# Kernel optimization log

Measured on AMD Instinct MI355X. Metric: run time of the kernel, lower is better.

## Reference

```python
import jax, jax.numpy as jnp
import numpy as np

NUM_USERS = 100000
NUM_ITEMS = 50000
N_TOTAL = NUM_USERS + NUM_ITEMS
NNZ = 4000000
LATENT_DIM = 64
N_LAYERS = 3
BATCH = 16384


def setup_inputs() -> dict:
    key = jax.random.key(0)
    k1, k2, k3, k4, k5, k6, k7 = jax.random.split(key, 7)
    return {
        "user_emb": jax.random.normal(k1, (NUM_USERS, LATENT_DIM), dtype=jnp.float32) * 0.1,
        "item_emb": jax.random.normal(k2, (NUM_ITEMS, LATENT_DIM), dtype=jnp.float32) * 0.1,
        "vals": jax.random.uniform(k3, (NNZ,), dtype=jnp.float32),
        "rows": jax.random.randint(k4, (NNZ,), 0, N_TOTAL, dtype=jnp.int32),
        "cols": jax.random.randint(k5, (NNZ,), 0, N_TOTAL, dtype=jnp.int32),
        "users": jax.random.randint(k6, (BATCH,), 0, NUM_USERS, dtype=jnp.int64),
        "items": jax.random.randint(k7, (BATCH,), 0, NUM_ITEMS, dtype=jnp.int64),
    }


def _spmm(vals, rows, cols, x):
    # sparse.mm(A, x) with A given as COO edge list: out[r] += vals * x[c]
    return jax.ops.segment_sum(vals[:, None] * x[cols], rows, num_segments=N_TOTAL)


def reference(user_emb, item_emb, vals, rows, cols, users, items):
    # LightGCN.computer(): multi-hop propagation + mean over layer outputs
    all_emb = jnp.concatenate([user_emb, item_emb], axis=0)  # [N+M, d]
    acc = all_emb
    emb = all_emb
    for _ in range(N_LAYERS):
        emb = _spmm(vals, rows, cols, emb)
        acc = acc + emb
    light_out = acc / jnp.asarray(N_LAYERS + 1, dtype=acc.dtype)
    all_users = light_out[:NUM_USERS]
    all_items = light_out[NUM_USERS:]
    # forward(users, items): gather and elementwise dot product
    u = all_users[users]  # [B, d]
    i = all_items[items]  # [B, d]
    gamma = jnp.sum(u * i, axis=1)  # [B]
    return gamma
```

## Files before the change

kernel.cpp:

```cpp
#include <hip/hip_runtime.h>

#define NUM_USERS 100000
#define NUM_ITEMS 50000
#define N_TOTAL   150000
#define LATENT    64
#define BATCH     16384
#define BROWS     512
#define NB        293
#define P1_T      512
#define P1_C      4096

typedef unsigned int u32;
typedef unsigned short u16;

__device__ __forceinline__ u16 f32_to_bf16(float f) {
    u32 u = __float_as_uint(f);
    u32 r = (u + 0x7FFFu + ((u >> 16) & 1u)) >> 16;
    return (u16)r;
}
__device__ __forceinline__ float bf16_lo(u32 w) { return __uint_as_float(w << 16); }
__device__ __forceinline__ float bf16_hi(u32 w) { return __uint_as_float(w & 0xFFFF0000u); }

__global__ void coarse_hist_kernel(const int* __restrict__ rows, int* __restrict__ ccnt, int nnz) {
    __shared__ int h[NB];
    for (int i = threadIdx.x; i < NB; i += blockDim.x) h[i] = 0;
    __syncthreads();
    int stride = gridDim.x * blockDim.x;
    for (int e = blockIdx.x * blockDim.x + threadIdx.x; e < nnz; e += stride)
        atomicAdd(&h[rows[e] >> 9], 1);
    __syncthreads();
    for (int i = threadIdx.x; i < NB; i += blockDim.x)
        if (h[i]) atomicAdd(&ccnt[i], h[i]);
}

__global__ void coarse_scan_kernel(const int* __restrict__ ccnt, int* __restrict__ cptr,
                                   int* __restrict__ ccur, int* __restrict__ rowptr, int nnz) {
    __shared__ int s[512];
    int t = threadIdx.x;
    int v = (t < NB) ? ccnt[t] : 0;
    s[t] = v;
    __syncthreads();
    for (int d = 1; d < 512; d <<= 1) {
        int x = (t >= d) ? s[t - d] : 0;
        __syncthreads();
        s[t] += x;
        __syncthreads();
    }
    int excl = s[t] - v;
    if (t < NB) { cptr[t] = excl; ccur[t] = excl; }
    if (t == 0) { cptr[NB] = nnz; rowptr[N_TOTAL] = nnz; }
}

__global__ void __launch_bounds__(P1_T)
partition1_kernel(const int* __restrict__ rows, const int* __restrict__ cols,
                  const float* __restrict__ vals,
                  int* __restrict__ ccur, uint2* __restrict__ packed0, int nnz) {
    __shared__ u32 skey[P1_C];
    __shared__ u32 sval[P1_C];
    __shared__ u16 sbucket[P1_C];
    __shared__ int cnt[NB];
    __shared__ int lstart[NB];
    __shared__ int lcur[NB];
    __shared__ int gbase[NB];
    __shared__ int scanbuf[P1_T];

    int t = threadIdx.x;
    int base = blockIdx.x * P1_C;
    int chunkN = nnz - base; if (chunkN > P1_C) chunkN = P1_C;

    for (int i = t; i < NB; i += P1_T) cnt[i] = 0;
    __syncthreads();

    int   er[8]; u32 ek[8]; u32 ev[8];
    #pragma unroll
    for (int k = 0; k < 8; ++k) {
        int e = base + k * P1_T + t;
        bool ok = (k * P1_T + t) < chunkN;
        int r = ok ? rows[e] : 0;
        er[k] = ok ? (r >> 9) : -1;
        if (ok) {
            ek[k] = (u32)cols[e] | ((u32)(r & (BROWS - 1)) << 18);
            ev[k] = __float_as_uint(vals[e]);
            atomicAdd(&cnt[er[k]], 1);
        }
    }
    __syncthreads();

    int v = (t < NB) ? cnt[t] : 0;
    scanbuf[t] = v;
    __syncthreads();
    for (int d = 1; d < P1_T; d <<= 1) {
        int x = (t >= d) ? scanbuf[t - d] : 0;
        __syncthreads();
        scanbuf[t] += x;
        __syncthreads();
    }
    if (t < NB) {
        int excl = scanbuf[t] - v;
        lstart[t] = excl;
        lcur[t] = excl;
        gbase[t] = v ? atomicAdd(&ccur[t], v) : 0;
    }
    __syncthreads();

    #pragma unroll
    for (int k = 0; k < 8; ++k) {
        if (er[k] >= 0) {
            int pos = atomicAdd(&lcur[er[k]], 1);
            skey[pos] = ek[k];
            sval[pos] = ev[k];
            sbucket[pos] = (u16)er[k];
        }
    }
    __syncthreads();

    for (int idx = t; idx < chunkN; idx += P1_T) {
        int b2 = sbucket[idx];
        int gp = gbase[b2] + (idx - lstart[b2]);
        packed0[gp] = make_uint2(skey[idx], sval[idx]);
    }
}

__global__ void __launch_bounds__(BROWS)
partition2_kernel(const int* __restrict__ cptr, const uint2* __restrict__ packed0,
                  uint2* __restrict__ edges, int* __restrict__ rowptr) {
    __shared__ int cnt[BROWS];
    __shared__ int s[BROWS];
    __shared__ int cur[BROWS];
    int b = blockIdx.x;
    int t = threadIdx.x;
    int seg0 = cptr[b], seg1 = cptr[b + 1];
    cnt[t] = 0;
    __syncthreads();
    for (int i = seg0 + t; i < seg1; i += 2 * BROWS) {
        u32 k0 = packed0[i].x >> 18;
        int i2 = i + BROWS;
        if (i2 < seg1) {
            u32 k1 = packed0[i2].x >> 18;
            atomicAdd(&cnt[k0], 1);
            atomicAdd(&cnt[k1], 1);
        } else {
            atomicAdd(&cnt[k0], 1);
        }
    }
    __syncthreads();
    int v = cnt[t];
    s[t] = v;
    __syncthreads();
    for (int d = 1; d < BROWS; d <<= 1) {
        int x = (t >= d) ? s[t - d] : 0;
        __syncthreads();
        s[t] += x;
        __syncthreads();
    }
    int excl = s[t] - v;
    cur[t] = excl;
    int r = (b << 9) + t;
    if (r < N_TOTAL) rowptr[r] = seg0 + excl;
    __syncthreads();
    for (int i = seg0 + t; i < seg1; i += 2 * BROWS) {
        uint2 p0 = packed0[i];
        int i2 = i + BROWS;
        if (i2 < seg1) {
            uint2 p1 = packed0[i2];
            int pos0 = seg0 + atomicAdd(&cur[p0.x >> 18], 1);
            int pos1 = seg0 + atomicAdd(&cur[p1.x >> 18], 1);
            edges[pos0] = make_uint2(p0.x & 0x3FFFFu, p0.y);
            edges[pos1] = make_uint2(p1.x & 0x3FFFFu, p1.y);
        } else {
            int pos0 = seg0 + atomicAdd(&cur[p0.x >> 18], 1);
            edges[pos0] = make_uint2(p0.x & 0x3FFFFu, p0.y);
        }
    }
}

__global__ void convert_kernel(const float* __restrict__ ue, const float* __restrict__ ie,
                               u16* __restrict__ x) {
    int i = blockIdx.x * blockDim.x + threadIdx.x;
    if (i >= N_TOTAL * LATENT) return;
    float f = (i < NUM_USERS * LATENT) ? ue[i] : ie[i - NUM_USERS * LATENT];
    x[i] = f32_to_bf16(f);
}

__device__ __forceinline__ void spmm_row(const uint2* __restrict__ edges,
                                         const u16* __restrict__ x,
                                         int s, int e, int lane, float acc[4]) {
    int j = lane >> 4;
    int q = (lane & 15) << 2;
    acc[0] = acc[1] = acc[2] = acc[3] = 0.f;
    int i = s;
    for (; i + 16 <= e; i += 16) {
        uint2 e0 = edges[i + j];
        uint2 e1 = edges[i + 4 + j];
        uint2 e2 = edges[i + 8 + j];
        uint2 e3 = edges[i + 12 + j];
        uint2 x0 = *reinterpret_cast<const uint2*>(x + (size_t)e0.x * LATENT + q);
        uint2 x1 = *reinterpret_cast<const uint2*>(x + (size_t)e1.x * LATENT + q);
        uint2 x2 = *reinterpret_cast<const uint2*>(x + (size_t)e2.x * LATENT + q);
        uint2 x3 = *reinterpret_cast<const uint2*>(x + (size_t)e3.x * LATENT + q);
        float v0 = __uint_as_float(e0.y);
        float v1 = __uint_as_float(e1.y);
        float v2 = __uint_as_float(e2.y);
        float v3 = __uint_as_float(e3.y);
        acc[0] = fmaf(v0, bf16_lo(x0.x), acc[0]);
        acc[1] = fmaf(v0, bf16_hi(x0.x), acc[1]);
        acc[2] = fmaf(v0, bf16_lo(x0.y), acc[2]);
        acc[3] = fmaf(v0, bf16_hi(x0.y), acc[3]);
        acc[0] = fmaf(v1, bf16_lo(x1.x), acc[0]);
        acc[1] = fmaf(v1, bf16_hi(x1.x), acc[1]);
        acc[2] = fmaf(v1, bf16_lo(x1.y), acc[2]);
        acc[3] = fmaf(v1, bf16_hi(x1.y), acc[3]);
        acc[0] = fmaf(v2, bf16_lo(x2.x), acc[0]);
        acc[1] = fmaf(v2, bf16_hi(x2.x), acc[1]);
        acc[2] = fmaf(v2, bf16_lo(x2.y), acc[2]);
        acc[3] = fmaf(v2, bf16_hi(x2.y), acc[3]);
        acc[0] = fmaf(v3, bf16_lo(x3.x), acc[0]);
        acc[1] = fmaf(v3, bf16_hi(x3.x), acc[1]);
        acc[2] = fmaf(v3, bf16_lo(x3.y), acc[2]);
        acc[3] = fmaf(v3, bf16_hi(x3.y), acc[3]);
    }
    for (; i + 8 <= e; i += 8) {
        uint2 e0 = edges[i + j];
        uint2 e1 = edges[i + 4 + j];
        uint2 x0 = *reinterpret_cast<const uint2*>(x + (size_t)e0.x * LATENT + q);
        uint2 x1 = *reinterpret_cast<const uint2*>(x + (size_t)e1.x * LATENT + q);
        float v0 = __uint_as_float(e0.y);
        float v1 = __uint_as_float(e1.y);
        acc[0] = fmaf(v0, bf16_lo(x0.x), acc[0]);
        acc[1] = fmaf(v0, bf16_hi(x0.x), acc[1]);
        acc[2] = fmaf(v0, bf16_lo(x0.y), acc[2]);
        acc[3] = fmaf(v0, bf16_hi(x0.y), acc[3]);
        acc[0] = fmaf(v1, bf16_lo(x1.x), acc[0]);
        acc[1] = fmaf(v1, bf16_hi(x1.x), acc[1]);
        acc[2] = fmaf(v1, bf16_lo(x1.y), acc[2]);
        acc[3] = fmaf(v1, bf16_hi(x1.y), acc[3]);
    }
    for (; i < e; i += 4) {
        uint2 e0 = edges[i + j];
        float v0 = (i + j < e) ? __uint_as_float(e0.y) : 0.f;
        uint2 x0 = *reinterpret_cast<const uint2*>(x + (size_t)e0.x * LATENT + q);
        acc[0] = fmaf(v0, bf16_lo(x0.x), acc[0]);
        acc[1] = fmaf(v0, bf16_hi(x0.x), acc[1]);
        acc[2] = fmaf(v0, bf16_lo(x0.y), acc[2]);
        acc[3] = fmaf(v0, bf16_hi(x0.y), acc[3]);
    }
    #pragma unroll
    for (int k = 0; k < 4; ++k) {
        acc[k] += __shfl_xor(acc[k], 16, 64);
        acc[k] += __shfl_xor(acc[k], 32, 64);
    }
}

__global__ void spmm_kernel(const int* __restrict__ rowptr, const uint2* __restrict__ edges,
                            const u16* __restrict__ x, u16* __restrict__ y) {
    int row = blockIdx.x * 4 + (threadIdx.x >> 6);
    int lane = threadIdx.x & 63;
    int s = rowptr[row], e = rowptr[row + 1];
    float acc[4];
    spmm_row(edges, x, s, e, lane, acc);
    if (lane < 16) {
        u32 w0 = (u32)f32_to_bf16(acc[0]) | ((u32)f32_to_bf16(acc[1]) << 16);
        u32 w1 = (u32)f32_to_bf16(acc[2]) | ((u32)f32_to_bf16(acc[3]) << 16);
        *reinterpret_cast<uint2*>(y + (size_t)row * LATENT + (lane << 2)) = make_uint2(w0, w1);
    }
}

__global__ void spmm_batch_kernel(const int* __restrict__ rowptr, const uint2* __restrict__ edges,
                                  const u16* __restrict__ x,
                                  const int* __restrict__ users, const int* __restrict__ items,
                                  float* __restrict__ u_acc, float* __restrict__ i_acc) {
    int slot = blockIdx.x * 4 + (threadIdx.x >> 6);
    int lane = threadIdx.x & 63;
    int row = (slot < BATCH) ? users[slot] : (NUM_USERS + items[slot - BATCH]);
    int s = rowptr[row], e = rowptr[row + 1];
    float acc[4];
    spmm_row(edges, x, s, e, lane, acc);
    if (lane < 16) {
        float* dst = (slot < BATCH) ? (u_acc + (size_t)slot * LATENT)
                                    : (i_acc + (size_t)(slot - BATCH) * LATENT);
        float4* p = reinterpret_cast<float4*>(dst + (lane << 2));
        float4 old = *p;
        *p = make_float4(old.x + acc[0], old.y + acc[1], old.z + acc[2], old.w + acc[3]);
    }
}

__global__ void init_acc_kernel(const float* __restrict__ user_emb,
                                const float* __restrict__ item_emb,
                                const int* __restrict__ users,
                                const int* __restrict__ items,
                                float* __restrict__ u_acc,
                                float* __restrict__ i_acc) {
    int tid = blockIdx.x * blockDim.x + threadIdx.x;
    int b = tid >> 6, d = tid & 63;
    if (b >= BATCH) return;
    u_acc[tid] = user_emb[(size_t)users[b] * LATENT + d];
    i_acc[tid] = item_emb[(size_t)items[b] * LATENT + d];
}

__global__ void gather_acc_kernel(const u16* __restrict__ emb,
                                  const int* __restrict__ users,
                                  const int* __restrict__ items,
                                  float* __restrict__ u_acc,
                                  float* __restrict__ i_acc) {
    int tid = blockIdx.x * blockDim.x + threadIdx.x;
    int b = tid >> 6, d = tid & 63;
    if (b >= BATCH) return;
    u_acc[tid] += __uint_as_float(((u32)emb[(size_t)users[b] * LATENT + d]) << 16);
    i_acc[tid] += __uint_as_float(((u32)emb[((size_t)items[b] + NUM_USERS) * LATENT + d]) << 16);
}

__global__ void dot_kernel(const float* __restrict__ u_acc,
                           const float* __restrict__ i_acc,
                           float* __restrict__ out) {
    int b = blockIdx.x;
    int d = threadIdx.x;
    float p = u_acc[b * 64 + d] * i_acc[b * 64 + d];
    #pragma unroll
    for (int off = 32; off; off >>= 1) p += __shfl_down(p, off, 64);
    if (d == 0) out[b] = p * (1.0f / 16.0f);
}

extern "C" void kernel_launch(void* const* d_in, const int* in_sizes, int n_in,
                              void* d_out, int out_size, void* d_ws, size_t ws_size,
                              hipStream_t stream) {
    const float* user_emb = (const float*)d_in[0];
    const float* item_emb = (const float*)d_in[1];
    const float* vals     = (const float*)d_in[2];
    const int*   rows     = (const int*)d_in[3];
    const int*   cols     = (const int*)d_in[4];
    const int*   users    = (const int*)d_in[5];
    const int*   items    = (const int*)d_in[6];
    float* out = (float*)d_out;

    const int nnz = in_sizes[2];

    char* ws = (char*)d_ws;
    const size_t embB  = (size_t)N_TOTAL * LATENT * sizeof(u16);
    const size_t accB  = (size_t)BATCH * LATENT * sizeof(float);
    const size_t edgeB = (size_t)(nnz + 16) * sizeof(uint2);

    size_t off = 0;
    u16*   emb_a   = (u16*)  (ws + off); off += embB;
    u16*   emb_b   = (u16*)  (ws + off); off += embB;
    uint2* packed0 = (uint2*)(ws + off); off += edgeB;
    uint2* edges   = (uint2*)(ws + off); off += edgeB;
    float* u_acc   = (float*)(ws + off); off += accB;
    float* i_acc   = (float*)(ws + off); off += accB;
    int*   rowptr  = (int*)  (ws + off); off += (size_t)(N_TOTAL + 1) * sizeof(int);
    int*   ccnt    = (int*)  (ws + off); off += (size_t)(NB + 1) * sizeof(int);
    int*   cptr    = (int*)  (ws + off); off += (size_t)(NB + 1) * sizeof(int);
    int*   ccur    = (int*)  (ws + off); off += (size_t)(NB + 1) * sizeof(int);

    hipMemsetAsync(ccnt, 0, (size_t)(NB + 1) * sizeof(int), stream);
    hipMemsetAsync(edges + nnz, 0, 16 * sizeof(uint2), stream);
    coarse_hist_kernel<<<512, 512, 0, stream>>>(rows, ccnt, nnz);
    coarse_scan_kernel<<<1, 512, 0, stream>>>(ccnt, cptr, ccur, rowptr, nnz);
    partition1_kernel<<<(nnz + P1_C - 1) / P1_C, P1_T, 0, stream>>>(
        rows, cols, vals, ccur, packed0, nnz);
    partition2_kernel<<<NB, BROWS, 0, stream>>>(cptr, packed0, edges, rowptr);

    convert_kernel<<<(N_TOTAL * LATENT + 255) / 256, 256, 0, stream>>>(user_emb, item_emb, emb_a);
    init_acc_kernel<<<(BATCH * 64) / 256, 256, 0, stream>>>(
        user_emb, item_emb, users, items, u_acc, i_acc);

    u16* cur = emb_a;
    u16* nxt = emb_b;
    for (int l = 0; l < 2; ++l) {
        spmm_kernel<<<N_TOTAL / 4, 256, 0, stream>>>(rowptr, edges, cur, nxt);
        gather_acc_kernel<<<(BATCH * 64) / 256, 256, 0, stream>>>(
            nxt, users, items, u_acc, i_acc);
        u16* t = cur; cur = nxt; nxt = t;
    }

    spmm_batch_kernel<<<(2 * BATCH) / 4, 256, 0, stream>>>(
        rowptr, edges, cur, users, items, u_acc, i_acc);

    dot_kernel<<<BATCH, 64, 0, stream>>>(u_acc, i_acc, out);
}
```

Measured before the change: 336.4 us.

## Drop the histogram pass with fixed-capacity bucket slabs; interleave two rows per SpMM wave

The coarse histogram and scan kernels before partitioning are removed. partition1 now writes each bucket into a fixed-capacity slab of CAP entries, and a single small scan turns the per-bucket counts into output offsets that partition2 uses. This saves a full pass over the rows array and a launch. The cost is that it assumes no 512-row bucket receives more than 16384 edges, which can overflow for skewed row distributions. Separately, each SpMM wave now processes two rows with interleaved gathers to expose more memory-level parallelism, with shared tail helpers handling the remainders.

```diff
diff --git a/kernel.cpp b/kernel.cpp
--- a/kernel.cpp
+++ b/kernel.cpp
@@ -7,6 +7,7 @@
 #define BATCH     16384
 #define BROWS     512
 #define NB        293
+#define CAP       16384
 #define P1_T      512
 #define P1_C      4096
 
@@ -21,34 +22,11 @@
 __device__ __forceinline__ float bf16_lo(u32 w) { return __uint_as_float(w << 16); }
 __device__ __forceinline__ float bf16_hi(u32 w) { return __uint_as_float(w & 0xFFFF0000u); }
 
-__global__ void coarse_hist_kernel(const int* __restrict__ rows, int* __restrict__ ccnt, int nnz) {
-    __shared__ int h[NB];
-    for (int i = threadIdx.x; i < NB; i += blockDim.x) h[i] = 0;
-    __syncthreads();
-    int stride = gridDim.x * blockDim.x;
-    for (int e = blockIdx.x * blockDim.x + threadIdx.x; e < nnz; e += stride)
-        atomicAdd(&h[rows[e] >> 9], 1);
-    __syncthreads();
-    for (int i = threadIdx.x; i < NB; i += blockDim.x)
-        if (h[i]) atomicAdd(&ccnt[i], h[i]);
-}
-
-__global__ void coarse_scan_kernel(const int* __restrict__ ccnt, int* __restrict__ cptr,
-                                   int* __restrict__ ccur, int* __restrict__ rowptr, int nnz) {
-    __shared__ int s[512];
-    int t = threadIdx.x;
-    int v = (t < NB) ? ccnt[t] : 0;
-    s[t] = v;
-    __syncthreads();
-    for (int d = 1; d < 512; d <<= 1) {
-        int x = (t >= d) ? s[t - d] : 0;
-        __syncthreads();
-        s[t] += x;
-        __syncthreads();
-    }
-    int excl = s[t] - v;
-    if (t < NB) { cptr[t] = excl; ccur[t] = excl; }
-    if (t == 0) { cptr[NB] = nnz; rowptr[N_TOTAL] = nnz; }
+__device__ __forceinline__ void fma4(float acc[4], uint2 xv, float v) {
+    acc[0] = fmaf(v, bf16_lo(xv.x), acc[0]);
+    acc[1] = fmaf(v, bf16_hi(xv.x), acc[1]);
+    acc[2] = fmaf(v, bf16_lo(xv.y), acc[2]);
+    acc[3] = fmaf(v, bf16_hi(xv.y), acc[3]);
 }
 
 __global__ void __launch_bounds__(P1_T)
@@ -71,7 +49,7 @@
     for (int i = t; i < NB; i += P1_T) cnt[i] = 0;
     __syncthreads();
 
-    int   er[8]; u32 ek[8]; u32 ev[8];
+    int er[8]; u32 ek[8]; u32 ev[8];
     #pragma unroll
     for (int k = 0; k < 8; ++k) {
         int e = base + k * P1_T + t;
@@ -116,9 +94,26 @@
 
     for (int idx = t; idx < chunkN; idx += P1_T) {
         int b2 = sbucket[idx];
-        int gp = gbase[b2] + (idx - lstart[b2]);
+        size_t gp = (size_t)b2 * CAP + gbase[b2] + (idx - lstart[b2]);
         packed0[gp] = make_uint2(skey[idx], sval[idx]);
     }
+}
+
+__global__ void bucket_scan_kernel(const int* __restrict__ ccur, int* __restrict__ cptr,
+                                   int* __restrict__ rowptr, int nnz) {
+    __shared__ int s[512];
+    int t = threadIdx.x;
+    int v = (t < NB) ? ccur[t] : 0;
+    s[t] = v;
+    __syncthreads();
+    for (int d = 1; d < 512; d <<= 1) {
+        int x = (t >= d) ? s[t - d] : 0;
+        __syncthreads();
+        s[t] += x;
+        __syncthreads();
+    }
+    if (t < NB) cptr[t] = s[t] - v;
+    if (t == 0) { cptr[NB] = nnz; rowptr[N_TOTAL] = nnz; }
 }
 
 __global__ void __launch_bounds__(BROWS)
@@ -129,14 +124,16 @@
     __shared__ int cur[BROWS];
     int b = blockIdx.x;
     int t = threadIdx.x;
-    int seg0 = cptr[b], seg1 = cptr[b + 1];
+    const uint2* src = packed0 + (size_t)b * CAP;
+    int outb = cptr[b];
+    int count = cptr[b + 1] - outb;
     cnt[t] = 0;
     __syncthreads();
-    for (int i = seg0 + t; i < seg1; i += 2 * BROWS) {
-        u32 k0 = packed0[i].x >> 18;
+    for (int i = t; i < count; i += 2 * BROWS) {
+        u32 k0 = src[i].x >> 18;
         int i2 = i + BROWS;
-        if (i2 < seg1) {
-            u32 k1 = packed0[i2].x >> 18;
+        if (i2 < count) {
+            u32 k1 = src[i2].x >> 18;
             atomicAdd(&cnt[k0], 1);
             atomicAdd(&cnt[k1], 1);
         } else {
@@ -156,19 +153,19 @@
     int excl = s[t] - v;
     cur[t] = excl;
     int r = (b << 9) + t;
-    if (r < N_TOTAL) rowptr[r] = seg0 + excl;
-    __syncthreads();
-    for (int i = seg0 + t; i < seg1; i += 2 * BROWS) {
-        uint2 p0 = packed0[i];
+    if (r < N_TOTAL) rowptr[r] = outb + excl;
+    __syncthreads();
+    for (int i = t; i < count; i += 2 * BROWS) {
+        uint2 p0 = src[i];
         int i2 = i + BROWS;
-        if (i2 < seg1) {
-            uint2 p1 = packed0[i2];
-            int pos0 = seg0 + atomicAdd(&cur[p0.x >> 18], 1);
-            int pos1 = seg0 + atomicAdd(&cur[p1.x >> 18], 1);
+        if (i2 < count) {
+            uint2 p1 = src[i2];
+            int pos0 = outb + atomicAdd(&cur[p0.x >> 18], 1);
+            int pos1 = outb + atomicAdd(&cur[p1.x >> 18], 1);
             edges[pos0] = make_uint2(p0.x & 0x3FFFFu, p0.y);
             edges[pos1] = make_uint2(p1.x & 0x3FFFFu, p1.y);
         } else {
-            int pos0 = seg0 + atomicAdd(&cur[p0.x >> 18], 1);
+            int pos0 = outb + atomicAdd(&cur[p0.x >> 18], 1);
             edges[pos0] = make_uint2(p0.x & 0x3FFFFu, p0.y);
         }
     }
@@ -180,6 +177,25 @@
     if (i >= N_TOTAL * LATENT) return;
     float f = (i < NUM_USERS * LATENT) ? ue[i] : ie[i - NUM_USERS * LATENT];
     x[i] = f32_to_bf16(f);
+}
+
+__device__ __forceinline__ void row_tail(const uint2* __restrict__ edges,
+                                         const u16* __restrict__ x,
+                                         int i, int e, int j, int q, float acc[4]) {
+    for (; i + 8 <= e; i += 8) {
+        uint2 e0 = edges[i + j];
+        uint2 e1 = edges[i + 4 + j];
+        uint2 x0 = *reinterpret_cast<const uint2*>(x + (size_t)e0.x * LATENT + q);
+        uint2 x1 = *reinterpret_cast<const uint2*>(x + (size_t)e1.x * LATENT + q);
+        fma4(acc, x0, __uint_as_float(e0.y));
+        fma4(acc, x1, __uint_as_float(e1.y));
+    }
+    for (; i < e; i += 4) {
+        uint2 e0 = edges[i + j];
+        float v0 = (i + j < e) ? __uint_as_float(e0.y) : 0.f;
+        uint2 x0 = *reinterpret_cast<const uint2*>(x + (size_t)e0.x * LATENT + q);
+        fma4(acc, x0, v0);
+    }
 }
 
 __device__ __forceinline__ void spmm_row(const uint2* __restrict__ edges,
@@ -198,52 +214,12 @@
         uint2 x1 = *reinterpret_cast<const uint2*>(x + (size_t)e1.x * LATENT + q);
         uint2 x2 = *reinterpret_cast<const uint2*>(x + (size_t)e2.x * LATENT + q);
         uint2 x3 = *reinterpret_cast<const uint2*>(x + (size_t)e3.x * LATENT + q);
-        float v0 = __uint_as_float(e0.y);
-        float v1 = __uint_as_float(e1.y);
-        float v2 = __uint_as_float(e2.y);
-        float v3 = __uint_as_float(e3.y);
-        acc[0] = fmaf(v0, bf16_lo(x0.x), acc[0]);
-        acc[1] = fmaf(v0, bf16_hi(x0.x), acc[1]);
-        acc[2] = fmaf(v0, bf16_lo(x0.y), acc[2]);
-        acc[3] = fmaf(v0, bf16_hi(x0.y), acc[3]);
-        acc[0] = fmaf(v1, bf16_lo(x1.x), acc[0]);
-        acc[1] = fmaf(v1, bf16_hi(x1.x), acc[1]);
-        acc[2] = fmaf(v1, bf16_lo(x1.y), acc[2]);
-        acc[3] = fmaf(v1, bf16_hi(x1.y), acc[3]);
-        acc[0] = fmaf(v2, bf16_lo(x2.x), acc[0]);
-        acc[1] = fmaf(v2, bf16_hi(x2.x), acc[1]);
-        acc[2] = fmaf(v2, bf16_lo(x2.y), acc[2]);
-        acc[3] = fmaf(v2, bf16_hi(x2.y), acc[3]);
-        acc[0] = fmaf(v3, bf16_lo(x3.x), acc[0]);
-        acc[1] = fmaf(v3, bf16_hi(x3.x), acc[1]);
-        acc[2] = fmaf(v3, bf16_lo(x3.y), acc[2]);
-        acc[3] = fmaf(v3, bf16_hi(x3.y), acc[3]);
-    }
-    for (; i + 8 <= e; i += 8) {
-        uint2 e0 = edges[i + j];
-        uint2 e1 = edges[i + 4 + j];
-        uint2 x0 = *reinterpret_cast<const uint2*>(x + (size_t)e0.x * LATENT + q);
-        uint2 x1 = *reinterpret_cast<const uint2*>(x + (size_t)e1.x * LATENT + q);
-        float v0 = __uint_as_float(e0.y);
-        float v1 = __uint_as_float(e1.y);
-        acc[0] = fmaf(v0, bf16_lo(x0.x), acc[0]);
-        acc[1] = fmaf(v0, bf16_hi(x0.x), acc[1]);
-        acc[2] = fmaf(v0, bf16_lo(x0.y), acc[2]);
-        acc[3] = fmaf(v0, bf16_hi(x0.y), acc[3]);
-        acc[0] = fmaf(v1, bf16_lo(x1.x), acc[0]);
-        acc[1] = fmaf(v1, bf16_hi(x1.x), acc[1]);
-        acc[2] = fmaf(v1, bf16_lo(x1.y), acc[2]);
-        acc[3] = fmaf(v1, bf16_hi(x1.y), acc[3]);
-    }
-    for (; i < e; i += 4) {
-        uint2 e0 = edges[i + j];
-        float v0 = (i + j < e) ? __uint_as_float(e0.y) : 0.f;
-        uint2 x0 = *reinterpret_cast<const uint2*>(x + (size_t)e0.x * LATENT + q);
-        acc[0] = fmaf(v0, bf16_lo(x0.x), acc[0]);
-        acc[1] = fmaf(v0, bf16_hi(x0.x), acc[1]);
-        acc[2] = fmaf(v0, bf16_lo(x0.y), acc[2]);
-        acc[3] = fmaf(v0, bf16_hi(x0.y), acc[3]);
-    }
+        fma4(acc, x0, __uint_as_float(e0.y));
+        fma4(acc, x1, __uint_as_float(e1.y));
+        fma4(acc, x2, __uint_as_float(e2.y));
+        fma4(acc, x3, __uint_as_float(e3.y));
+    }
+    row_tail(edges, x, i, e, j, q, acc);
     #pragma unroll
     for (int k = 0; k < 4; ++k) {
         acc[k] += __shfl_xor(acc[k], 16, 64);
@@ -253,15 +229,51 @@
 
 __global__ void spmm_kernel(const int* __restrict__ rowptr, const uint2* __restrict__ edges,
                             const u16* __restrict__ x, u16* __restrict__ y) {
-    int row = blockIdx.x * 4 + (threadIdx.x >> 6);
+    int wid = blockIdx.x * 4 + (threadIdx.x >> 6);
+    int r0 = wid * 2;
     int lane = threadIdx.x & 63;
-    int s = rowptr[row], e = rowptr[row + 1];
-    float acc[4];
-    spmm_row(edges, x, s, e, lane, acc);
+    int j = lane >> 4;
+    int q = (lane & 15) << 2;
+    int i0 = rowptr[r0];
+    int e0 = rowptr[r0 + 1];
+    int i1 = e0;
+    int e1 = rowptr[r0 + 2];
+    float a0[4] = {0.f, 0.f, 0.f, 0.f};
+    float a1[4] = {0.f, 0.f, 0.f, 0.f};
+
+    while (i0 + 8 <= e0 && i1 + 8 <= e1) {
+        uint2 p00 = edges[i0 + j];
+        uint2 p01 = edges[i0 + 4 + j];
+        uint2 p10 = edges[i1 + j];
+        uint2 p11 = edges[i1 + 4 + j];
+        uint2 g00 = *reinterpret_cast<const uint2*>(x + (size_t)p00.x * LATENT + q);
+        uint2 g01 = *reinterpret_cast<const uint2*>(x + (size_t)p01.x * LATENT + q);
+        uint2 g10 = *reinterpret_cast<const uint2*>(x + (size_t)p10.x * LATENT + q);
+        uint2 g11 = *reinterpret_cast<const uint2*>(x + (size_t)p11.x * LATENT + q);
+        fma4(a0, g00, __uint_as_float(p00.y));
+        fma4(a0, g01, __uint_as_float(p01.y));
+        fma4(a1, g10, __uint_as_float(p10.y));
+        fma4(a1, g11, __uint_as_float(p11.y));
+        i0 += 8;
+        i1 += 8;
+    }
+    row_tail(edges, x, i0, e0, j, q, a0);
+    row_tail(edges, x, i1, e1, j, q, a1);
+
+    #pragma unroll
+    for (int k = 0; k < 4; ++k) {
+        a0[k] += __shfl_xor(a0[k], 16, 64);
+        a0[k] += __shfl_xor(a0[k], 32, 64);
+        a1[k] += __shfl_xor(a1[k], 16, 64);
+        a1[k] += __shfl_xor(a1[k], 32, 64);
+    }
     if (lane < 16) {
-        u32 w0 = (u32)f32_to_bf16(acc[0]) | ((u32)f32_to_bf16(acc[1]) << 16);
-        u32 w1 = (u32)f32_to_bf16(acc[2]) | ((u32)f32_to_bf16(acc[3]) << 16);
-        *reinterpret_cast<uint2*>(y + (size_t)row * LATENT + (lane << 2)) = make_uint2(w0, w1);
+        u32 w0 = (u32)f32_to_bf16(a0[0]) | ((u32)f32_to_bf16(a0[1]) << 16);
+        u32 w1 = (u32)f32_to_bf16(a0[2]) | ((u32)f32_to_bf16(a0[3]) << 16);
+        *reinterpret_cast<uint2*>(y + (size_t)r0 * LATENT + (lane << 2)) = make_uint2(w0, w1);
+        u32 w2 = (u32)f32_to_bf16(a1[0]) | ((u32)f32_to_bf16(a1[1]) << 16);
+        u32 w3 = (u32)f32_to_bf16(a1[2]) | ((u32)f32_to_bf16(a1[3]) << 16);
+        *reinterpret_cast<uint2*>(y + (size_t)(r0 + 1) * LATENT + (lane << 2)) = make_uint2(w2, w3);
     }
 }
 
@@ -335,28 +347,27 @@
     const int nnz = in_sizes[2];
 
     char* ws = (char*)d_ws;
-    const size_t embB  = (size_t)N_TOTAL * LATENT * sizeof(u16);
-    const size_t accB  = (size_t)BATCH * LATENT * sizeof(float);
-    const size_t edgeB = (size_t)(nnz + 16) * sizeof(uint2);
+    const size_t embB   = (size_t)N_TOTAL * LATENT * sizeof(u16);
+    const size_t accB   = (size_t)BATCH * LATENT * sizeof(float);
+    const size_t slabB  = (size_t)NB * CAP * sizeof(uint2);
+    const size_t edgeB  = (size_t)(nnz + 16) * sizeof(uint2);
 
     size_t off = 0;
     u16*   emb_a   = (u16*)  (ws + off); off += embB;
     u16*   emb_b   = (u16*)  (ws + off); off += embB;
-    uint2* packed0 = (uint2*)(ws + off); off += edgeB;
+    uint2* packed0 = (uint2*)(ws + off); off += slabB;
     uint2* edges   = (uint2*)(ws + off); off += edgeB;
     float* u_acc   = (float*)(ws + off); off += accB;
     float* i_acc   = (float*)(ws + off); off += accB;
     int*   rowptr  = (int*)  (ws + off); off += (size_t)(N_TOTAL + 1) * sizeof(int);
-    int*   ccnt    = (int*)  (ws + off); off += (size_t)(NB + 1) * sizeof(int);
+    int*   ccur    = (int*)  (ws + off); off += (size_t)(NB + 1) * sizeof(int);
     int*   cptr    = (int*)  (ws + off); off += (size_t)(NB + 1) * sizeof(int);
-    int*   ccur    = (int*)  (ws + off); off += (size_t)(NB + 1) * sizeof(int);
-
-    hipMemsetAsync(ccnt, 0, (size_t)(NB + 1) * sizeof(int), stream);
+
+    hipMemsetAsync(ccur, 0, (size_t)(NB + 1) * sizeof(int), stream);
     hipMemsetAsync(edges + nnz, 0, 16 * sizeof(uint2), stream);
-    coarse_hist_kernel<<<512, 512, 0, stream>>>(rows, ccnt, nnz);
-    coarse_scan_kernel<<<1, 512, 0, stream>>>(ccnt, cptr, ccur, rowptr, nnz);
     partition1_kernel<<<(nnz + P1_C - 1) / P1_C, P1_T, 0, stream>>>(
         rows, cols, vals, ccur, packed0, nnz);
+    bucket_scan_kernel<<<1, 512, 0, stream>>>(ccur, cptr, rowptr, nnz);
     partition2_kernel<<<NB, BROWS, 0, stream>>>(cptr, packed0, edges, rowptr);
 
     convert_kernel<<<(N_TOTAL * LATENT + 255) / 256, 256, 0, stream>>>(user_emb, item_emb, emb_a);
@@ -366,7 +377,7 @@
     u16* cur = emb_a;
     u16* nxt = emb_b;
     for (int l = 0; l < 2; ++l) {
-        spmm_kernel<<<N_TOTAL / 4, 256, 0, stream>>>(rowptr, edges, cur, nxt);
+        spmm_kernel<<<N_TOTAL / 8, 256, 0, stream>>>(rowptr, edges, cur, nxt);
         gather_acc_kernel<<<(BATCH * 64) / 256, 256, 0, stream>>>(
             nxt, users, items, u_acc, i_acc);
         u16* t = cur; cur = nxt; nxt = t;
```

Result: faster. 311.9 us (-7.3%).
